# Kernel tuning notes

Hardware: AMD Instinct MI355X
Metric: run time of the kernel (lower is better)

Reference implementation:

```python
import jax, jax.numpy as jnp
import numpy as np

B, F, V, D = 4096, 24, 1000, 32
RED = 8            # max(1, F // 3) SENet bottleneck
COMB = 2 * F * D   # 1536
EPS = 1e-5


def setup_inputs() -> dict:
    key = jax.random.key(0)
    ks = jax.random.split(key, 12)
    return {
        "x": jax.random.randint(ks[0], (B, F), 0, V),
        "emb_tables": jax.random.normal(ks[1], (F, V, D), jnp.float32) * 0.05,
        "lin_tables": jax.random.normal(ks[2], (F, V), jnp.float32) * 0.05,
        "bias": jnp.zeros((1,), jnp.float32),
        "se_w1": jax.random.normal(ks[3], (RED, F), jnp.float32) * 0.2,
        "se_w2": jax.random.normal(ks[4], (F, RED), jnp.float32) * 0.2,
        "bil_W": jax.random.normal(ks[5], (F, F, D, D), jnp.float32) * (1.0 / np.sqrt(D)),
        "w0": jax.random.normal(ks[6], (COMB, 1024), jnp.float32) * 0.02,
        "b0": jnp.zeros((1024,), jnp.float32),
        "g0": jnp.ones((1024,), jnp.float32),
        "be0": jnp.zeros((1024,), jnp.float32),
        "w1": jax.random.normal(ks[7], (1024, 512), jnp.float32) * 0.02,
        "b1": jnp.zeros((512,), jnp.float32),
        "g1": jnp.ones((512,), jnp.float32),
        "be1": jnp.zeros((512,), jnp.float32),
        "w2": jax.random.normal(ks[8], (512, 1), jnp.float32) * 0.02,
        "b2": jnp.zeros((1,), jnp.float32),
    }


def _bilinear_field_interaction(e, W):
    # e: [B,F,D], W: [F,F,D,D]
    # out[b,i,k] = e[b,i,k] * sum_{j != i} (W[i,j] @ e[b,j])[k]
    t = jnp.einsum('ijkl,bjl->bijk', W, e)          # [B,F,F,D]
    mask = 1.0 - jnp.eye(F, dtype=e.dtype)          # zero the i==j terms
    s = jnp.einsum('bijk,ij->bik', t, mask)         # [B,F,D]
    return e * s


def _senet(e, w1, w2):
    Z = e.mean(axis=2)                              # [B,F] squeeze
    A = jax.nn.sigmoid(jax.nn.relu(Z @ w1.T) @ w2.T)  # [B,F]
    return e * A[:, :, None]


def _bn_train(h, g, b):
    m = h.mean(axis=0)
    v = h.var(axis=0)  # biased, matches torch BN normalization
    return g * (h - m) * jax.lax.rsqrt(v + EPS) + b


def reference(x, emb_tables, lin_tables, bias, se_w1, se_w2, bil_W,
              w0, b0, g0, be0, w1, b1, g1, be1, w2, b2):
    fidx = jnp.arange(F)[None, :]                   # [1,F]
    emb = emb_tables[fidx, x]                       # [B,F,D]
    lin = lin_tables[fidx, x].sum(axis=1)           # [B] first-order term

    se_emb = _senet(emb, se_w1, se_w2)
    p = _bilinear_field_interaction(emb, bil_W)     # [B,F,D]
    q = _bilinear_field_interaction(se_emb, bil_W)  # [B,F,D]
    combined = jnp.concatenate(
        [p.reshape(B, F * D), q.reshape(B, F * D)], axis=1)  # [B,2FD]

    h = jax.nn.relu(_bn_train(combined @ w0 + b0, g0, be0))
    h = jax.nn.relu(_bn_train(h @ w1 + b1, g1, be1))
    mlp_out = (h @ w2 + b2)[:, 0]                   # [B]

    logit = lin + bias[0] + mlp_out
    return jax.nn.sigmoid(logit)                    # [B]
```

## Files before the change

kernel.cpp:

```cpp
#include <hip/hip_runtime.h>

#define B_SZ 4096
#define F_SZ 24
#define V_SZ 1000
#define D_SZ 32
#define RED  8
#define FD   768
#define COMB 1536
#define H0   1024
#define H1   512
#define EPS  1e-5f

typedef __bf16 bf16x8 __attribute__((ext_vector_type(8)));
typedef float  f32x4  __attribute__((ext_vector_type(4)));
typedef const __attribute__((address_space(1))) unsigned int* gptr_t;
typedef       __attribute__((address_space(3))) unsigned int* lptr_t;

__device__ __forceinline__ float bf2f(unsigned short u) {
    union { unsigned int i; float f; } v; v.i = ((unsigned int)u) << 16; return v.f;
}
__device__ __forceinline__ unsigned short f2bf(float f) {
    union { float f; unsigned int i; } v; v.f = f;
    unsigned int u = v.i;
    return (unsigned short)((u + 0x7FFFu + ((u >> 16) & 1u)) >> 16);
}
__device__ __forceinline__ unsigned int pack2(float a, float b) {
    return (unsigned int)f2bf(a) | ((unsigned int)f2bf(b) << 16);
}

__global__ __launch_bounds__(256) void prep_gather(
        const int* __restrict__ x, const float* __restrict__ emb,
        const float* __restrict__ lint, const float* __restrict__ sw1,
        const float* __restrict__ sw2, const float* __restrict__ bw,
        const float* __restrict__ w0, const float* __restrict__ w1,
        unsigned short* __restrict__ Xbf, unsigned short* __restrict__ Wt,
        unsigned short* __restrict__ w0t, unsigned short* __restrict__ w1t,
        float* __restrict__ lin, float* __restrict__ sums) {
    int bid = blockIdx.x;
    int tid = threadIdx.x;
    if (bid < 1024) {
        int w = tid >> 6, lane = tid & 63;
        int b = bid * 4 + w;
        __shared__ int   xi[4][F_SZ];
        __shared__ float e[4][F_SZ][D_SZ];
        __shared__ float Z[4][F_SZ];
        __shared__ float r1[4][RED];
        __shared__ float Afac[4][F_SZ];
        if (lane < F_SZ) xi[w][lane] = x[b * F_SZ + lane];
        __syncthreads();
        #pragma unroll
        for (int it = 0; it < 3; it++) {
            int idx = it * 64 + lane;
            int f = idx >> 3, k4 = (idx & 7) * 4;
            float4 v = *(const float4*)&emb[((size_t)f * V_SZ + xi[w][f]) * D_SZ + k4];
            *(float4*)&e[w][f][k4] = v;
        }
        __syncthreads();
        if (lane < F_SZ) {
            float s = 0.f;
            #pragma unroll
            for (int k = 0; k < D_SZ; k++) s += e[w][lane][k];
            Z[w][lane] = s * (1.f / D_SZ);
        }
        __syncthreads();
        if (lane < RED) {
            float s = 0.f;
            #pragma unroll
            for (int f = 0; f < F_SZ; f++) s += Z[w][f] * sw1[lane * F_SZ + f];
            r1[w][lane] = fmaxf(s, 0.f);
        }
        __syncthreads();
        if (lane < F_SZ) {
            float s = 0.f;
            #pragma unroll
            for (int r = 0; r < RED; r++) s += r1[w][r] * sw2[lane * RED + r];
            Afac[w][lane] = 1.f / (1.f + expf(-s));
        }
        __syncthreads();
        #pragma unroll
        for (int it = 0; it < 3; it++) {
            int idx = it * 64 + lane;
            int f = idx >> 3, k4 = (idx & 7) * 4;
            const float* p = &e[w][f][k4];
            uint2 u, us;
            u.x = pack2(p[0], p[1]); u.y = pack2(p[2], p[3]);
            float a = Afac[w][f];
            us.x = pack2(p[0] * a, p[1] * a); us.y = pack2(p[2] * a, p[3] * a);
            *(uint2*)&Xbf[(size_t)b * FD + idx * 4] = u;
            *(uint2*)&Xbf[(size_t)(B_SZ + b) * FD + idx * 4] = us;
        }
        float lv = (lane < F_SZ) ? lint[lane * V_SZ + xi[w][lane]] : 0.f;
        #pragma unroll
        for (int off = 32; off > 0; off >>= 1) lv += __shfl_down(lv, off);
        if (lane == 0) lin[b] = lv;
    } else if (bid < 3328) {
        int o = (bid - 1024) * 256 + tid;
        int ik = o / FD, jl = o - ik * FD;
        int i = ik >> 5, k = ik & 31, j = jl >> 5, l = jl & 31;
        Wt[o] = (i == j) ? (unsigned short)0
                         : f2bf(bw[(((size_t)i * F_SZ + j) * D_SZ + k) * D_SZ + l]);
    } else if (bid < 5376) {
        __shared__ float tile[32][33];
        const float* in; unsigned short* out; int K, N, bx, by;
        if (bid < 4864) { int t = bid - 3328; in = w0; out = w0t; K = COMB; N = H0; bx = t & 31; by = t >> 5; }
        else            { int t = bid - 4864; in = w1; out = w1t; K = H0;   N = H1; bx = t & 15; by = t >> 4; }
        int tx = tid & 31, ty = tid >> 5;
        int n0 = bx * 32, k0 = by * 32;
        #pragma unroll
        for (int r = 0; r < 32; r += 8)
            tile[ty + r][tx] = in[(size_t)(k0 + ty + r) * N + n0 + tx];
        __syncthreads();
        #pragma unroll
        for (int r = 0; r < 32; r += 8)
            out[(size_t)(n0 + ty + r) * K + k0 + tx] = f2bf(tile[tx][ty + r]);
    } else {
        int o = (bid - 5376) * 256 + tid;
        sums[o] = 0.f;
    }
}

template<int MODE, int K, int N, int TM, int TN>
__global__ __launch_bounds__(256) void mfma_gemm(
        const unsigned short* __restrict__ A,
        const unsigned short* __restrict__ Bt,
        const float* __restrict__ bias,
        const unsigned short* __restrict__ Xbf,
        unsigned short* __restrict__ Obf,
        float* __restrict__ sum, float* __restrict__ sumsq) {
    constexpr int MI = TM / 32, NI = TN / 32;
    __shared__ unsigned short Abuf[TM * 32];
    __shared__ unsigned short Bbuf[TN * 32];
    const int tid  = threadIdx.x;
    const int lane = tid & 63, wv = tid >> 6;
    const int wm = (wv >> 1) * (TM / 2), wn = (wv & 1) * (TN / 2);
    const int fr = lane & 15, kq = lane >> 4;
    const int bm = blockIdx.y * TM, bn = blockIdx.x * TN;
    const int srow = tid >> 2;
    const int skc  = (tid & 3) * 8;

    f32x4 acc[MI][NI];
    #pragma unroll
    for (int i = 0; i < MI; i++)
        #pragma unroll
        for (int j = 0; j < NI; j++) {
            f32x4 z = {0.f, 0.f, 0.f, 0.f};
            acc[i][j] = z;
        }

    for (int k0 = 0; k0 < K; k0 += 32) {
        #pragma unroll
        for (int c = 0; c < TM / 64; c++) {
            const unsigned short* ga = A + (size_t)(bm + c * 64 + srow) * K + k0 + skc;
            char* la = (char*)Abuf + c * 4096 + wv * 1024;
            __builtin_amdgcn_global_load_lds((gptr_t)ga, (lptr_t)la, 16, 0, 0);
        }
        #pragma unroll
        for (int c = 0; c < TN / 64; c++) {
            const unsigned short* gb = Bt + (size_t)(bn + c * 64 + srow) * K + k0 + skc;
            char* lb = (char*)Bbuf + c * 4096 + wv * 1024;
            __builtin_amdgcn_global_load_lds((gptr_t)gb, (lptr_t)lb, 16, 0, 0);
        }
        __syncthreads();
        bf16x8 af[MI], bfv[NI];
        #pragma unroll
        for (int mi = 0; mi < MI; mi++)
            af[mi] = *(const bf16x8*)&Abuf[(wm + mi * 16 + fr) * 32 + kq * 8];
        #pragma unroll
        for (int ni = 0; ni < NI; ni++)
            bfv[ni] = *(const bf16x8*)&Bbuf[(wn + ni * 16 + fr) * 32 + kq * 8];
        #pragma unroll
        for (int mi = 0; mi < MI; mi++)
            #pragma unroll
            for (int ni = 0; ni < NI; ni++)
                acc[mi][ni] = __builtin_amdgcn_mfma_f32_16x16x32_bf16(
                    af[mi], bfv[ni], acc[mi][ni], 0, 0, 0);
        __syncthreads();
    }

    if (MODE == 0) {
        #pragma unroll
        for (int mi = 0; mi < MI; mi++)
            #pragma unroll
            for (int ni = 0; ni < NI; ni++) {
                int col = bn + wn + ni * 16 + fr;
                #pragma unroll
                for (int r = 0; r < 4; r++) {
                    int row = bm + wm + mi * 16 + kq * 4 + r;
                    float xv = bf2f(Xbf[(size_t)row * FD + col]);
                    float cv = xv * acc[mi][ni][r];
                    size_t off = (row < B_SZ)
                        ? ((size_t)row * COMB + col)
                        : ((size_t)(row - B_SZ) * COMB + FD + col);
                    Obf[off] = f2bf(cv);
                }
            }
    } else {
        #pragma unroll
        for (int ni = 0; ni < NI; ni++) {
            int col = bn + wn + ni * 16 + fr;
            float bv = bias[col];
            float s = 0.f, ss = 0.f;
            #pragma unroll
            for (int mi = 0; mi < MI; mi++)
                #pragma unroll
                for (int r = 0; r < 4; r++) {
                    int row = bm + wm + mi * 16 + kq * 4 + r;
                    float v = acc[mi][ni][r] + bv;
                    Obf[(size_t)row * N + col] = f2bf(v);
                    s += v; ss += v * v;
                }
            s  += __shfl_xor(s, 16);  s  += __shfl_xor(s, 32);
            ss += __shfl_xor(ss, 16); ss += __shfl_xor(ss, 32);
            if (kq == 0) {
                atomicAdd(&sum[col], s);
                atomicAdd(&sumsq[col], ss);
            }
        }
    }
}

__global__ __launch_bounds__(256) void bn_apply(const unsigned short* __restrict__ h,
        const float* __restrict__ sum, const float* __restrict__ sumsq,
        const float* __restrict__ g, const float* __restrict__ be,
        unsigned short* __restrict__ out) {
    __shared__ float sc_s[128], sh_s[128];
    int cb = blockIdx.x & 7, rb = blockIdx.x >> 3;
    int c0 = cb * 128, r0 = rb * 64;
    int t = threadIdx.x;
    if (t < 128) {
        int c = c0 + t;
        float m = sum[c] * (1.f / B_SZ);
        float var = sumsq[c] * (1.f / B_SZ) - m * m;
        float rstd = rsqrtf(var + EPS);
        float sc = g[c] * rstd;
        sc_s[t] = sc;
        sh_s[t] = be[c] - m * sc;
    }
    __syncthreads();
    int lc = (t & 15) * 8;
    int lr = t >> 4;
    #pragma unroll
    for (int p = 0; p < 4; p++) {
        int row = r0 + p * 16 + lr;
        size_t base = (size_t)row * H0 + c0 + lc;
        uint4 hv = *(const uint4*)&h[base];
        unsigned int uu[4] = {hv.x, hv.y, hv.z, hv.w};
        unsigned int oo[4];
        #pragma unroll
        for (int q = 0; q < 4; q++) {
            int cc = lc + 2 * q;
            float v0 = bf2f((unsigned short)(uu[q] & 0xFFFF)) * sc_s[cc] + sh_s[cc];
            float v1 = bf2f((unsigned short)(uu[q] >> 16)) * sc_s[cc + 1] + sh_s[cc + 1];
            oo[q] = pack2(fmaxf(v0, 0.f), fmaxf(v1, 0.f));
        }
        uint4 ov; ov.x = oo[0]; ov.y = oo[1]; ov.z = oo[2]; ov.w = oo[3];
        *(uint4*)&out[base] = ov;
    }
}

__global__ __launch_bounds__(256) void final_k(const unsigned short* __restrict__ h1,
        const float* __restrict__ sum, const float* __restrict__ sumsq,
        const float* __restrict__ g, const float* __restrict__ be,
        const float* __restrict__ w2, const float* __restrict__ b2,
        const float* __restrict__ lin, const float* __restrict__ bias,
        float* __restrict__ out) {
    __shared__ float sc_s[H1], sh_s[H1], w2_s[H1];
    int t = threadIdx.x;
    int wv = t >> 6, lane = t & 63;
    #pragma unroll
    for (int q = 0; q < 2; q++) {
        int c = q * 256 + t;
        float m = sum[c] * (1.f / B_SZ);
        float var = sumsq[c] * (1.f / B_SZ) - m * m;
        float rstd = rsqrtf(var + EPS);
        float sc = g[c] * rstd;
        sc_s[c] = sc;
        sh_s[c] = be[c] - m * sc;
        w2_s[c] = w2[c];
    }
    __syncthreads();
    int r0 = blockIdx.x * 16;
    #pragma unroll
    for (int i = 0; i < 4; i++) {
        int row = r0 + wv * 4 + i;
        int c0 = lane * 8;
        uint4 hv = *(const uint4*)&h1[(size_t)row * H1 + c0];
        unsigned int uu[4] = {hv.x, hv.y, hv.z, hv.w};
        float acc = 0.f;
        #pragma unroll
        for (int q = 0; q < 4; q++) {
            int c = c0 + 2 * q;
            float v0 = bf2f((unsigned short)(uu[q] & 0xFFFF)) * sc_s[c] + sh_s[c];
            float v1 = bf2f((unsigned short)(uu[q] >> 16)) * sc_s[c + 1] + sh_s[c + 1];
            acc += fmaxf(v0, 0.f) * w2_s[c] + fmaxf(v1, 0.f) * w2_s[c + 1];
        }
        #pragma unroll
        for (int off = 32; off > 0; off >>= 1) acc += __shfl_down(acc, off);
        if (lane == 0) {
            float logit = lin[row] + bias[0] + acc + b2[0];
            out[row] = 1.f / (1.f + expf(-logit));
        }
    }
}

extern "C" void kernel_launch(void* const* d_in, const int* in_sizes, int n_in,
                              void* d_out, int out_size, void* d_ws, size_t ws_size,
                              hipStream_t stream) {
    const int*   x    = (const int*)d_in[0];
    const float* emb  = (const float*)d_in[1];
    const float* lint = (const float*)d_in[2];
    const float* bias = (const float*)d_in[3];
    const float* sw1  = (const float*)d_in[4];
    const float* sw2  = (const float*)d_in[5];
    const float* bw   = (const float*)d_in[6];
    const float* w0   = (const float*)d_in[7];
    const float* b0   = (const float*)d_in[8];
    const float* g0   = (const float*)d_in[9];
    const float* be0  = (const float*)d_in[10];
    const float* w1   = (const float*)d_in[11];
    const float* b1   = (const float*)d_in[12];
    const float* g1   = (const float*)d_in[13];
    const float* be1  = (const float*)d_in[14];
    const float* w2   = (const float*)d_in[15];
    const float* b2   = (const float*)d_in[16];
    float* out = (float*)d_out;

    char* p = (char*)d_ws;
    auto alloc = [&](size_t bytes) { char* r = p; p += (bytes + 255) & ~(size_t)255; return r; };

    unsigned short* Xbf  = (unsigned short*)alloc((size_t)2 * B_SZ * FD * 2);
    unsigned short* Wt   = (unsigned short*)alloc((size_t)FD * FD * 2);
    unsigned short* w0t  = (unsigned short*)alloc((size_t)H0 * COMB * 2);
    unsigned short* w1t  = (unsigned short*)alloc((size_t)H1 * H0 * 2);
    unsigned short* Cbf  = (unsigned short*)alloc((size_t)B_SZ * COMB * 2);
    unsigned short* h0bf = (unsigned short*)alloc((size_t)B_SZ * H0 * 2);
    unsigned short* A2bf = (unsigned short*)alloc((size_t)B_SZ * H0 * 2);
    unsigned short* h1bf = (unsigned short*)alloc((size_t)B_SZ * H1 * 2);
    float* lin = (float*)alloc(B_SZ * 4);
    float* sums = (float*)alloc((2 * H0 + 2 * H1) * 4);
    float* sum0 = sums, *sumsq0 = sums + H0, *sum1 = sums + 2 * H0, *sumsq1 = sums + 2 * H0 + H1;

    prep_gather<<<5388, 256, 0, stream>>>(x, emb, lint, sw1, sw2, bw, w0, w1,
                                          Xbf, Wt, w0t, w1t, lin, sums);

    mfma_gemm<0, FD, FD, 128, 64><<<dim3(FD / 64, 2 * B_SZ / 128), 256, 0, stream>>>(
        Xbf, Wt, nullptr, Xbf, Cbf, nullptr, nullptr);
    mfma_gemm<1, COMB, H0, 128, 64><<<dim3(H0 / 64, B_SZ / 128), 256, 0, stream>>>(
        Cbf, w0t, b0, nullptr, h0bf, sum0, sumsq0);
    bn_apply<<<512, 256, 0, stream>>>(h0bf, sum0, sumsq0, g0, be0, A2bf);
    mfma_gemm<1, H0, H1, 64, 64><<<dim3(H1 / 64, B_SZ / 64), 256, 0, stream>>>(
        A2bf, w1t, b1, nullptr, h1bf, sum1, sumsq1);
    final_k<<<B_SZ / 16, 256, 0, stream>>>(h1bf, sum1, sumsq1, g1, be1,
                                           w2, b2, lin, bias, out);
}
```

Measured before the change: 179.9 us.

## Fuse BN0 apply and ReLU into second MLP GEMM A-load; remap blocks per XCD

Removes the separate bn_apply kernel and its intermediate buffer. The second MLP GEMM now computes the BN scale and shift from the column sums, then normalizes and applies ReLU while loading A tiles into shared memory. This trades the async global-to-LDS copy for a register-path load plus per-element math in that GEMM. All GEMMs also switch to a 1D grid with an XCD-aware block-to-tile mapping, which groups row blocks per XCD for L2 locality.

```diff
diff --git a/kernel.cpp b/kernel.cpp
--- a/kernel.cpp
+++ b/kernel.cpp
@@ -119,24 +119,46 @@
     }
 }
 
-template<int MODE, int K, int N, int TM, int TN>
+template<int MODE, int K, int N, int TM, int TN, int GX, int GY>
 __global__ __launch_bounds__(256) void mfma_gemm(
         const unsigned short* __restrict__ A,
         const unsigned short* __restrict__ Bt,
         const float* __restrict__ bias,
         const unsigned short* __restrict__ Xbf,
         unsigned short* __restrict__ Obf,
-        float* __restrict__ sum, float* __restrict__ sumsq) {
+        float* __restrict__ sum, float* __restrict__ sumsq,
+        const float* __restrict__ psum, const float* __restrict__ psumsq,
+        const float* __restrict__ g, const float* __restrict__ be) {
     constexpr int MI = TM / 32, NI = TN / 32;
     __shared__ unsigned short Abuf[TM * 32];
     __shared__ unsigned short Bbuf[TN * 32];
+    __shared__ float sc_s[MODE == 2 ? K : 1];
+    __shared__ float sh_s[MODE == 2 ? K : 1];
     const int tid  = threadIdx.x;
     const int lane = tid & 63, wv = tid >> 6;
     const int wm = (wv >> 1) * (TM / 2), wn = (wv & 1) * (TN / 2);
     const int fr = lane & 15, kq = lane >> 4;
-    const int bm = blockIdx.y * TM, bn = blockIdx.x * TN;
+    const int bid = blockIdx.x;
+    const int xcd = bid & 7, slot = bid >> 3;
+    const int rowb = xcd * (GY / 8) + slot / GX;
+    const int colb = slot % GX;
+    const int bm = rowb * TM, bn = colb * TN;
     const int srow = tid >> 2;
     const int skc  = (tid & 3) * 8;
+
+    if (MODE == 2) {
+        #pragma unroll
+        for (int q = 0; q < K / 256; q++) {
+            int c = q * 256 + tid;
+            float m = psum[c] * (1.f / B_SZ);
+            float var = psumsq[c] * (1.f / B_SZ) - m * m;
+            float rstd = rsqrtf(var + EPS);
+            float sc = g[c] * rstd;
+            sc_s[c] = sc;
+            sh_s[c] = be[c] - m * sc;
+        }
+        __syncthreads();
+    }
 
     f32x4 acc[MI][NI];
     #pragma unroll
@@ -148,11 +170,26 @@
         }
 
     for (int k0 = 0; k0 < K; k0 += 32) {
-        #pragma unroll
-        for (int c = 0; c < TM / 64; c++) {
-            const unsigned short* ga = A + (size_t)(bm + c * 64 + srow) * K + k0 + skc;
-            char* la = (char*)Abuf + c * 4096 + wv * 1024;
-            __builtin_amdgcn_global_load_lds((gptr_t)ga, (lptr_t)la, 16, 0, 0);
+        if (MODE == 2) {
+            uint4 hv = *(const uint4*)&A[(size_t)(bm + srow) * K + k0 + skc];
+            unsigned int uu[4] = {hv.x, hv.y, hv.z, hv.w};
+            unsigned int oo[4];
+            #pragma unroll
+            for (int q = 0; q < 4; q++) {
+                int c = k0 + skc + 2 * q;
+                float v0 = bf2f((unsigned short)(uu[q] & 0xFFFF)) * sc_s[c] + sh_s[c];
+                float v1 = bf2f((unsigned short)(uu[q] >> 16)) * sc_s[c + 1] + sh_s[c + 1];
+                oo[q] = pack2(fmaxf(v0, 0.f), fmaxf(v1, 0.f));
+            }
+            uint4 ov; ov.x = oo[0]; ov.y = oo[1]; ov.z = oo[2]; ov.w = oo[3];
+            *(uint4*)&Abuf[srow * 32 + skc] = ov;
+        } else {
+            #pragma unroll
+            for (int c = 0; c < TM / 64; c++) {
+                const unsigned short* ga = A + (size_t)(bm + c * 64 + srow) * K + k0 + skc;
+                char* la = (char*)Abuf + c * 4096 + wv * 1024;
+                __builtin_amdgcn_global_load_lds((gptr_t)ga, (lptr_t)la, 16, 0, 0);
+            }
         }
         #pragma unroll
         for (int c = 0; c < TN / 64; c++) {
@@ -216,45 +253,6 @@
                 atomicAdd(&sumsq[col], ss);
             }
         }
-    }
-}
-
-__global__ __launch_bounds__(256) void bn_apply(const unsigned short* __restrict__ h,
-        const float* __restrict__ sum, const float* __restrict__ sumsq,
-        const float* __restrict__ g, const float* __restrict__ be,
-        unsigned short* __restrict__ out) {
-    __shared__ float sc_s[128], sh_s[128];
-    int cb = blockIdx.x & 7, rb = blockIdx.x >> 3;
-    int c0 = cb * 128, r0 = rb * 64;
-    int t = threadIdx.x;
-    if (t < 128) {
-        int c = c0 + t;
-        float m = sum[c] * (1.f / B_SZ);
-        float var = sumsq[c] * (1.f / B_SZ) - m * m;
-        float rstd = rsqrtf(var + EPS);
-        float sc = g[c] * rstd;
-        sc_s[t] = sc;
-        sh_s[t] = be[c] - m * sc;
-    }
-    __syncthreads();
-    int lc = (t & 15) * 8;
-    int lr = t >> 4;
-    #pragma unroll
-    for (int p = 0; p < 4; p++) {
-        int row = r0 + p * 16 + lr;
-        size_t base = (size_t)row * H0 + c0 + lc;
-        uint4 hv = *(const uint4*)&h[base];
-        unsigned int uu[4] = {hv.x, hv.y, hv.z, hv.w};
-        unsigned int oo[4];
-        #pragma unroll
-        for (int q = 0; q < 4; q++) {
-            int cc = lc + 2 * q;
-            float v0 = bf2f((unsigned short)(uu[q] & 0xFFFF)) * sc_s[cc] + sh_s[cc];
-            float v1 = bf2f((unsigned short)(uu[q] >> 16)) * sc_s[cc + 1] + sh_s[cc + 1];
-            oo[q] = pack2(fmaxf(v0, 0.f), fmaxf(v1, 0.f));
-        }
-        uint4 ov; ov.x = oo[0]; ov.y = oo[1]; ov.z = oo[2]; ov.w = oo[3];
-        *(uint4*)&out[base] = ov;
     }
 }
 
@@ -334,7 +332,6 @@
     unsigned short* w1t  = (unsigned short*)alloc((size_t)H1 * H0 * 2);
     unsigned short* Cbf  = (unsigned short*)alloc((size_t)B_SZ * COMB * 2);
     unsigned short* h0bf = (unsigned short*)alloc((size_t)B_SZ * H0 * 2);
-    unsigned short* A2bf = (unsigned short*)alloc((size_t)B_SZ * H0 * 2);
     unsigned short* h1bf = (unsigned short*)alloc((size_t)B_SZ * H1 * 2);
     float* lin = (float*)alloc(B_SZ * 4);
     float* sums = (float*)alloc((2 * H0 + 2 * H1) * 4);
@@ -343,13 +340,12 @@
     prep_gather<<<5388, 256, 0, stream>>>(x, emb, lint, sw1, sw2, bw, w0, w1,
                                           Xbf, Wt, w0t, w1t, lin, sums);
 
-    mfma_gemm<0, FD, FD, 128, 64><<<dim3(FD / 64, 2 * B_SZ / 128), 256, 0, stream>>>(
-        Xbf, Wt, nullptr, Xbf, Cbf, nullptr, nullptr);
-    mfma_gemm<1, COMB, H0, 128, 64><<<dim3(H0 / 64, B_SZ / 128), 256, 0, stream>>>(
-        Cbf, w0t, b0, nullptr, h0bf, sum0, sumsq0);
-    bn_apply<<<512, 256, 0, stream>>>(h0bf, sum0, sumsq0, g0, be0, A2bf);
-    mfma_gemm<1, H0, H1, 64, 64><<<dim3(H1 / 64, B_SZ / 64), 256, 0, stream>>>(
-        A2bf, w1t, b1, nullptr, h1bf, sum1, sumsq1);
+    mfma_gemm<0, FD, FD, 128, 64, 12, 64><<<768, 256, 0, stream>>>(
+        Xbf, Wt, nullptr, Xbf, Cbf, nullptr, nullptr, nullptr, nullptr, nullptr, nullptr);
+    mfma_gemm<1, COMB, H0, 128, 64, 16, 32><<<512, 256, 0, stream>>>(
+        Cbf, w0t, b0, nullptr, h0bf, sum0, sumsq0, nullptr, nullptr, nullptr, nullptr);
+    mfma_gemm<2, H0, H1, 64, 64, 8, 64><<<512, 256, 0, stream>>>(
+        h0bf, w1t, b1, nullptr, h1bf, sum1, sumsq1, sum0, sumsq0, g0, be0);
     final_k<<<B_SZ / 16, 256, 0, stream>>>(h1bf, sum1, sumsq1, g1, be1,
                                            w2, b2, lin, bias, out);
 }
```

After: 177.3 us. No clear change (-1.4%).
